# Performance work log

Hardware: AMD Instinct MI355X
Metric: run time of the kernel (lower is better)

The kernel has to match this reference:

```python
import jax, jax.numpy as jnp
import numpy as np

B, T = 2, 1000
IN_DIM, OUT_DIM = 257, 514
D_MODEL, D_STATE, D_CONV, EXPAND = 512, 16, 4, 2
D_INNER = EXPAND * D_MODEL          # 1024
DT_RANK = (D_MODEL + 15) // 16      # ceil(512/16) = 32
N_LAYER = 4
K_DC = 31                            # depthwise conv kernel in MambaDCLayer


def layer_norm(x, g, b, eps=1e-5):
    mu = jnp.mean(x, axis=-1, keepdims=True)
    var = jnp.mean((x - mu) ** 2, axis=-1, keepdims=True)
    return (x - mu) * jax.lax.rsqrt(var + eps) * g + b


def dw_conv1d(x, w, b, pad):
    # x: (B, T, C), w: (C, K) depthwise, pad: (left, right)
    y = jax.lax.conv_general_dilated(
        x.transpose(0, 2, 1), w[:, None, :], (1,), [pad],
        dimension_numbers=('NCH', 'OIH', 'NCH'), feature_group_count=w.shape[0])
    return (y + b[None, :, None]).transpose(0, 2, 1)


def mamba_block(x, W_in, conv_w, conv_b, W_x, W_dt, b_dt, A_log, Dp, W_out):
    # x: (B, T, d_model)
    xz = x @ W_in                               # (B, T, 2*D_INNER)
    xin, z = jnp.split(xz, 2, axis=-1)
    xin = dw_conv1d(xin, conv_w, conv_b, (D_CONV - 1, 0))  # causal depthwise conv
    xin = jax.nn.silu(xin)                      # (B, T, D_INNER)
    proj = xin @ W_x                            # (B, T, DT_RANK + 2*D_STATE)
    dt = jax.nn.softplus(proj[..., :DT_RANK] @ W_dt + b_dt)  # (B, T, D_INNER)
    Bm = proj[..., DT_RANK:DT_RANK + D_STATE]   # (B, T, D_STATE)
    Cm = proj[..., DT_RANK + D_STATE:]          # (B, T, D_STATE)
    A = -jnp.exp(A_log)                         # (D_INNER, D_STATE)
    dA = jnp.exp(dt[..., None] * A)             # (B, T, D_INNER, D_STATE)
    dBu = (dt * xin)[..., None] * Bm[:, :, None, :]  # (B, T, D_INNER, D_STATE)

    def step(h, inp):
        dA_t, dBu_t, C_t = inp
        h = dA_t * h + dBu_t
        return h, jnp.einsum('bds,bs->bd', h, C_t)

    h0 = jnp.zeros((x.shape[0], D_INNER, D_STATE), x.dtype)
    _, ys = jax.lax.scan(step, h0, (dA.transpose(1, 0, 2, 3),
                                    dBu.transpose(1, 0, 2, 3),
                                    Cm.transpose(1, 0, 2)))
    y = ys.transpose(1, 0, 2) + xin * Dp        # (B, T, D_INNER)
    y = y * jax.nn.silu(z)
    return y @ W_out                            # (B, T, d_model)


def setup_inputs() -> dict:
    key = jax.random.key(0)
    ks = iter(jax.random.split(key, 32))
    n = lambda shape, s=0.02: jax.random.normal(next(ks), shape, jnp.float32) * s
    return {
        'x': jax.random.normal(next(ks), (B, T, IN_DIM), jnp.float32),
        'lengths': jnp.full((B,), T, jnp.int32),
        'w_in0': n((IN_DIM, D_MODEL)),
        'ln_in_g': jnp.ones((D_MODEL,), jnp.float32),
        'ln_in_b': jnp.zeros((D_MODEL,), jnp.float32),
        'ln1_g': jnp.ones((N_LAYER, D_MODEL), jnp.float32),
        'ln1_b': jnp.zeros((N_LAYER, D_MODEL), jnp.float32),
        'W_inproj': n((N_LAYER, D_MODEL, 2 * D_INNER)),
        'conv_w': n((N_LAYER, D_INNER, D_CONV), 0.1),
        'conv_b': jnp.zeros((N_LAYER, D_INNER), jnp.float32),
        'W_xproj': n((N_LAYER, D_INNER, DT_RANK + 2 * D_STATE)),
        'W_dt': n((N_LAYER, DT_RANK, D_INNER), 0.1),
        'b_dt': jnp.full((N_LAYER, D_INNER), -4.6, jnp.float32),
        'A_log': jnp.tile(jnp.log(jnp.arange(1, D_STATE + 1, dtype=jnp.float32)),
                          (N_LAYER, D_INNER, 1)),
        'D': jnp.ones((N_LAYER, D_INNER), jnp.float32),
        'W_mo': n((N_LAYER, D_INNER, D_MODEL)),
        'ln2_g': jnp.ones((N_LAYER, D_MODEL), jnp.float32),
        'ln2_b': jnp.zeros((N_LAYER, D_MODEL), jnp.float32),
        'dc_w': n((N_LAYER, D_MODEL, K_DC), 0.1),
        'dc_b': jnp.zeros((N_LAYER, D_MODEL), jnp.float32),
        'w_out': n((D_MODEL, OUT_DIM)),
        'b_out': jnp.zeros((OUT_DIM,), jnp.float32),
    }


def reference(x, lengths, w_in0, ln_in_g, ln_in_b, ln1_g, ln1_b, W_inproj,
              conv_w, conv_b, W_xproj, W_dt, b_dt, A_log, D, W_mo,
              ln2_g, ln2_b, dc_w, dc_b, w_out, b_out):
    seq_mask = jnp.arange(x.shape[1]) < lengths[:, None]  # (B, T) bool
    h = jax.nn.relu(layer_norm(x @ w_in0, ln_in_g, ln_in_b))
    for i in range(N_LAYER):
        a = h + mamba_block(layer_norm(h, ln1_g[i], ln1_b[i]),
                            W_inproj[i], conv_w[i], conv_b[i], W_xproj[i],
                            W_dt[i], b_dt[i], A_log[i], D[i], W_mo[i])
        c = dw_conv1d(layer_norm(a, ln2_g[i], ln2_b[i]), dc_w[i], dc_b[i],
                      (K_DC // 2, K_DC // 2))  # 'same' padding
        h = a + c
    out = h @ w_out + b_out  # MagcIRM -> linear output head
    # lengths == T so output[seq_mask] is a full flatten to (B*T, OUT_DIM)
    out_flat = out.reshape(-1, out.shape[-1])
    return out_flat, seq_mask
```

## Files before the change

### kernel.cpp

```cpp
#include <hip/hip_runtime.h>
#include <cstdint>
#include <cstddef>

#define DEVI static __device__ __forceinline__

typedef unsigned short ushort_t;
typedef __attribute__((ext_vector_type(8))) short short8;
typedef __attribute__((ext_vector_type(4))) float f32x4;

DEVI float sp_softplus(float x) { return x > 20.f ? x : log1pf(__expf(x)); }
DEVI float silu_f(float x)      { return x / (1.f + __expf(-x)); }

DEVI ushort_t f2b(float v) {
    uint32_t u = __builtin_bit_cast(uint32_t, v);
    u += 0x7FFFu + ((u >> 16) & 1u);
    return (ushort_t)(u >> 16);
}
DEVI float b2f(ushort_t u) {
    uint32_t x = ((uint32_t)u) << 16;
    return __builtin_bit_cast(float, x);
}

DEVI void gload16(const ushort_t* g, ushort_t* l) {
    __builtin_amdgcn_global_load_lds(
        (const __attribute__((address_space(1))) unsigned int*)g,
        (__attribute__((address_space(3))) unsigned int*)l, 16, 0, 0);
}

#define NC 40
#define CL 25

template<bool RELU, bool OUTB16>
__global__ __launch_bounds__(256) void ln_k(const float* __restrict__ x,
                                            const float* __restrict__ g,
                                            const float* __restrict__ b,
                                            void* __restrict__ yv, int M)
{
    int wid  = threadIdx.x >> 6;
    int lane = threadIdx.x & 63;
    int row  = blockIdx.x * 4 + wid;
    if (row >= M) return;
    const float* xr = x + (size_t)row * 512;
    float4 v0 = *(const float4*)(xr + lane * 8);
    float4 v1 = *(const float4*)(xr + lane * 8 + 4);
    float vals[8] = {v0.x, v0.y, v0.z, v0.w, v1.x, v1.y, v1.z, v1.w};
    float s = 0.f;
#pragma unroll
    for (int i = 0; i < 8; i++) s += vals[i];
#pragma unroll
    for (int off = 1; off < 64; off <<= 1) s += __shfl_xor(s, off);
    float mu = s * (1.f / 512.f);
    float q = 0.f;
#pragma unroll
    for (int i = 0; i < 8; i++) { float d = vals[i] - mu; q += d * d; }
#pragma unroll
    for (int off = 1; off < 64; off <<= 1) q += __shfl_xor(q, off);
    float rstd = rsqrtf(q * (1.f / 512.f) + 1e-5f);
#pragma unroll
    for (int i = 0; i < 8; i++) {
        int c = lane * 8 + i;
        float o = (vals[i] - mu) * rstd * g[c] + b[c];
        if (RELU) o = fmaxf(o, 0.f);
        if (OUTB16) ((ushort_t*)yv)[(size_t)row * 512 + c] = f2b(o);
        else        ((float*)yv)[(size_t)row * 512 + c] = o;
    }
}

__global__ __launch_bounds__(256) void prep_all_k(const float* __restrict__ conv_w,
                                                  const float* __restrict__ dc_w,
                                                  const float* __restrict__ x,
                                                  float* __restrict__ cwt,
                                                  float* __restrict__ dcwt,
                                                  ushort_t* __restrict__ xb)
{
    int e = blockIdx.x * 256 + threadIdx.x;
    if (e < 16384) {
        int l = e >> 12, rem = e & 4095, k = rem >> 10, d = rem & 1023;
        cwt[e] = conv_w[l * 4096 + d * 4 + k];
        return;
    }
    e -= 16384;
    if (e < 63488) {
        int l = e / 15872, rem = e % 15872, k = rem / 512, m = rem % 512;
        dcwt[e] = dc_w[l * 15872 + m * 31 + k];
        return;
    }
    e -= 63488;
    if (e < 2000 * 320) {
        int k = e % 320, row = e / 320;
        xb[e] = (k < 257) ? f2b(x[(size_t)row * 257 + k]) : (ushort_t)0;
    }
}

__global__ __launch_bounds__(256) void tr_w_k(const float* __restrict__ src,
                                              ushort_t* __restrict__ dst,
                                              int Ktrue, int N, int ldo, int srcld,
                                              size_t sstride, size_t dstride)
{
    __shared__ float tile[32][33];
    src += blockIdx.z * sstride;
    dst += blockIdx.z * dstride;
    int n0 = blockIdx.x * 32, k0 = blockIdx.y * 32;
    int tx = threadIdx.x & 31, ty = threadIdx.x >> 5;
#pragma unroll
    for (int r = 0; r < 4; r++) {
        int k = k0 + ty + r * 8, n = n0 + tx;
        tile[ty + r * 8][tx] = (k < Ktrue && n < N) ? src[(size_t)k * srcld + n] : 0.f;
    }
    __syncthreads();
#pragma unroll
    for (int r = 0; r < 4; r++) {
        int n = n0 + ty + r * 8;
        if (n < N) dst[(size_t)n * ldo + k0 + tx] = f2b(tile[tx][ty + r * 8]);
    }
}

template<bool BIAS, int ACT, bool RES, bool OUTF32, bool OUTB16>
__global__ __launch_bounds__(256) void gemm7(
    const ushort_t* __restrict__ A, int lda,
    const ushort_t* __restrict__ Bt, int ldb,
    const float* __restrict__ bias,
    const float* __restrict__ R, int ldr,
    float* __restrict__ C, int ldc,
    ushort_t* __restrict__ C2, int ldc2,
    int M, int N, int K,
    size_t aStr, size_t bStr, size_t cStr)
{
    __shared__ ushort_t As[3 * 4096];
    __shared__ ushort_t Bs[3 * 4096];
    A  += blockIdx.z * aStr;
    Bt += blockIdx.z * bStr;
    C  += blockIdx.z * cStr;
    C2 += blockIdx.z * cStr;

    int tid = threadIdx.x;
    int wid = tid >> 6, l = tid & 63;
    int wr = wid >> 1, wc = wid & 1;
    int lk = l >> 4, lr = l & 15;
    int rhalf = tid >> 3, oct = tid & 7;

    int nwg = gridDim.x * gridDim.y;
    int bid = blockIdx.y * gridDim.x + blockIdx.x;
    {
        int q = nwg >> 3, r = nwg & 7;
        int xcd = bid & 7, lo = bid >> 3;
        bid = (xcd < r ? xcd * (q + 1) : r * (q + 1) + (xcd - r) * q) + lo;
    }
    int bx = bid % gridDim.x, by = bid / gridDim.x;
    int bm = by * 64, bn = bx * 64;

    int cg = oct ^ (rhalf & 7);
    const ushort_t* aS0 = A  + (size_t)(bm + rhalf) * lda + cg * 8;
    const ushort_t* aS1 = aS0 + (size_t)32 * lda;
    const ushort_t* bS0 = Bt + (size_t)(bn + rhalf) * ldb + cg * 8;
    const ushort_t* bS1 = bS0 + (size_t)32 * ldb;

    int rowA = wr * 32 + lr;
    int colB = wc * 32 + lr;
    int a0 = rowA * 64 + ((0 + lk) ^ (rowA & 7)) * 8;
    int a1 = rowA * 64 + ((4 + lk) ^ (rowA & 7)) * 8;
    int b0 = colB * 64 + ((0 + lk) ^ (colB & 7)) * 8;
    int b1 = colB * 64 + ((4 + lk) ^ (colB & 7)) * 8;

    f32x4 acc00 = {0.f,0.f,0.f,0.f}, acc01 = {0.f,0.f,0.f,0.f};
    f32x4 acc10 = {0.f,0.f,0.f,0.f}, acc11 = {0.f,0.f,0.f,0.f};

#define STAGE(B_) do { \
        gload16(aS0, &As[(B_) * 4096 + tid * 8]); \
        gload16(aS1, &As[(B_) * 4096 + 2048 + tid * 8]); \
        gload16(bS0, &Bs[(B_) * 4096 + tid * 8]); \
        gload16(bS1, &Bs[(B_) * 4096 + 2048 + tid * 8]); \
        aS0 += 64; aS1 += 64; bS0 += 64; bS1 += 64; \
    } while (0)

#define COMPUTE(B_) do { \
        short8 af0 = *(const short8*)&As[(B_) * 4096 + a0]; \
        short8 af1 = *(const short8*)&As[(B_) * 4096 + 1024 + a0]; \
        short8 bf0 = *(const short8*)&Bs[(B_) * 4096 + b0]; \
        short8 bf1 = *(const short8*)&Bs[(B_) * 4096 + 1024 + b0]; \
        acc00 = __builtin_amdgcn_mfma_f32_16x16x32_bf16(af0, bf0, acc00, 0, 0, 0); \
        acc01 = __builtin_amdgcn_mfma_f32_16x16x32_bf16(af0, bf1, acc01, 0, 0, 0); \
        acc10 = __builtin_amdgcn_mfma_f32_16x16x32_bf16(af1, bf0, acc10, 0, 0, 0); \
        acc11 = __builtin_amdgcn_mfma_f32_16x16x32_bf16(af1, bf1, acc11, 0, 0, 0); \
        af0 = *(const short8*)&As[(B_) * 4096 + a1]; \
        af1 = *(const short8*)&As[(B_) * 4096 + 1024 + a1]; \
        bf0 = *(const short8*)&Bs[(B_) * 4096 + b1]; \
        bf1 = *(const short8*)&Bs[(B_) * 4096 + 1024 + b1]; \
        acc00 = __builtin_amdgcn_mfma_f32_16x16x32_bf16(af0, bf0, acc00, 0, 0, 0); \
        acc01 = __builtin_amdgcn_mfma_f32_16x16x32_bf16(af0, bf1, acc01, 0, 0, 0); \
        acc10 = __builtin_amdgcn_mfma_f32_16x16x32_bf16(af1, bf0, acc10, 0, 0, 0); \
        acc11 = __builtin_amdgcn_mfma_f32_16x16x32_bf16(af1, bf1, acc11, 0, 0, 0); \
    } while (0)

#define STEP(T_, B_) do { \
        if ((T_) + 1 < nt) asm volatile("s_waitcnt vmcnt(4)" ::: "memory"); \
        else               asm volatile("s_waitcnt vmcnt(0)" ::: "memory"); \
        __builtin_amdgcn_s_barrier(); \
        if ((T_) + 2 < nt) STAGE(((B_) + 2) % 3); \
        COMPUTE(B_); \
    } while (0)

    int nt = K >> 6;
    STAGE(0);
    if (nt > 1) STAGE(1);
    int t = 0;
    for (; t + 3 <= nt; t += 3) { STEP(t, 0); STEP(t + 1, 1); STEP(t + 2, 2); }
    if (t < nt) { STEP(t, 0); t++; }
    if (t < nt) { STEP(t, 1); }

#undef STAGE
#undef COMPUTE
#undef STEP

    f32x4 accs[2][2] = {{acc00, acc01}, {acc10, acc11}};
#pragma unroll
    for (int m = 0; m < 2; m++) {
#pragma unroll
        for (int n = 0; n < 2; n++) {
            int gn = bn + wc * 32 + n * 16 + lr;
            if (gn >= N) continue;
#pragma unroll
            for (int r = 0; r < 4; r++) {
                int gm = bm + wr * 32 + m * 16 + lk * 4 + r;
                if (gm >= M) continue;
                float v = accs[m][n][r];
                if (ACT == 3) {
                    if (gn < 32) C2[(size_t)gm * ldc2 + gn] = f2b(v);
                    else { C[(size_t)gm * ldc + gn] = v;
                           C2[(size_t)gm * ldc2 + gn] = 0; }
                    continue;
                }
                if (BIAS) v += bias[gn];
                if (ACT == 1) v = sp_softplus(v);
                if (RES) v += R[(size_t)gm * ldr + gn];
                if (OUTF32) C[(size_t)gm * ldc + gn] = v;
                if (OUTB16) C2[(size_t)gm * ldc2 + gn] = f2b(v);
            }
        }
    }
}

__global__ __launch_bounds__(256) void conv4_silu_k(const ushort_t* __restrict__ xzb,
                                                    const float* __restrict__ cwt,
                                                    const float* __restrict__ bias,
                                                    ushort_t* __restrict__ xinb)
{
    int e = blockIdx.x * 256 + threadIdx.x;
    if (e >= 2000 * 128) return;
    int dg = (e & 127) * 8;
    int row = e >> 7;
    int b = row >= 1000 ? 1 : 0;
    int t = row - b * 1000;
    float acc[8];
#pragma unroll
    for (int j = 0; j < 8; j++) acc[j] = bias[dg + j];
#pragma unroll
    for (int k = 0; k < 4; k++) {
        int tt = t - 3 + k;
        if (tt < 0) continue;
        short8 v = *(const short8*)&xzb[(size_t)(b * 1000 + tt) * 2048 + dg];
#pragma unroll
        for (int j = 0; j < 8; j++)
            acc[j] += b2f((ushort_t)v[j]) * cwt[k * 1024 + dg + j];
    }
    short8 o;
#pragma unroll
    for (int j = 0; j < 8; j++) o[j] = (short)f2b(silu_f(acc[j]));
    *(short8*)&xinb[(size_t)row * 1024 + dg] = o;
}

__global__ __launch_bounds__(256) void scan_part1(const ushort_t* __restrict__ dt,
                                                  const ushort_t* __restrict__ xin,
                                                  const float* __restrict__ proj,
                                                  const float* __restrict__ A_log,
                                                  float* __restrict__ hloc,
                                                  float* __restrict__ sc)
{
    __shared__ ushort_t s_dt[CL][64], s_x[CL][64];
    __shared__ float s_B[CL][16];
    int d0 = blockIdx.x * 64;
    int c  = blockIdx.y;
    int b  = blockIdx.z;
    int tid = threadIdx.x;
    int ch = tid >> 2, st4 = tid & 3;
    int d = d0 + ch;
    int base = b * 1000 + c * CL;
    for (int lin = tid; lin < CL * 8; lin += 256) {
        int r = lin >> 3, q = lin & 7;
        size_t row = (size_t)(base + r);
        *(short8*)&s_dt[r][q * 8] = *(const short8*)&dt[row * 1024 + d0 + q * 8];
        *(short8*)&s_x[r][q * 8]  = *(const short8*)&xin[row * 1024 + d0 + q * 8];
    }
    for (int lin = tid; lin < CL * 16; lin += 256) {
        int r = lin >> 4, j = lin & 15;
        s_B[r][j] = proj[(size_t)(base + r) * 64 + 32 + j];
    }
    float4 alog = *(const float4*)&A_log[d * 16 + st4 * 4];
    float a_s[4] = {-__expf(alog.x), -__expf(alog.y), -__expf(alog.z), -__expf(alog.w)};
    __syncthreads();
    float h[4] = {0.f, 0.f, 0.f, 0.f};
    float sdt = 0.f;
#pragma unroll 5
    for (int t = 0; t < CL; t++) {
        float dtv = b2f(s_dt[t][ch]);
        float xv  = b2f(s_x[t][ch]);
        float4 Bv = *(const float4*)&s_B[t][st4 * 4];
        float dx = dtv * xv;
        sdt += dtv;
        h[0] = __expf(dtv * a_s[0]) * h[0] + dx * Bv.x;
        h[1] = __expf(dtv * a_s[1]) * h[1] + dx * Bv.y;
        h[2] = __expf(dtv * a_s[2]) * h[2] + dx * Bv.z;
        h[3] = __expf(dtv * a_s[3]) * h[3] + dx * Bv.w;
    }
    *(float4*)&hloc[((size_t)(b * NC + c) << 14) + ((size_t)d << 4) + st4 * 4] =
        (float4){h[0], h[1], h[2], h[3]};
    if (st4 == 0) sc[(b * NC + c) * 1024 + d] = sdt;
}

__global__ __launch_bounds__(256) void scan_combine(const float* __restrict__ A_log,
                                                    float* __restrict__ hloc,
                                                    const float* __restrict__ sc)
{
    int e = blockIdx.x * 256 + threadIdx.x;
    if (e >= 2 * 16384) return;
    int b = e >> 14;
    int rem = e & 16383;
    int dd = rem >> 4;
    float a_s = -__expf(A_log[rem]);
    float H = hloc[((size_t)(b * NC) << 14) + rem];
    for (int c = 1; c < NC; c++) {
        size_t idx = ((size_t)(b * NC + c) << 14) + rem;
        H = hloc[idx] + __expf(a_s * sc[(b * NC + c) * 1024 + dd]) * H;
        hloc[idx] = H;
    }
}

__global__ __launch_bounds__(256) void scan_part2(const ushort_t* __restrict__ dt,
                                                  const ushort_t* __restrict__ xin,
                                                  const float* __restrict__ proj,
                                                  const float* __restrict__ A_log,
                                                  const float* __restrict__ hend,
                                                  const float* __restrict__ Dp,
                                                  const ushort_t* __restrict__ xzb,
                                                  ushort_t* __restrict__ ysb)
{
    __shared__ ushort_t s_dt[CL][64], s_x[CL][64], s_y[CL][64];
    __shared__ float s_B[CL][16], s_C[CL][16];
    __shared__ float s_Dp[64];
    int d0 = blockIdx.x * 64;
    int c  = blockIdx.y;
    int b  = blockIdx.z;
    int tid = threadIdx.x;
    int ch = tid >> 2, st4 = tid & 3;
    int d = d0 + ch;
    int base = b * 1000 + c * CL;
    if (tid < 64) s_Dp[tid] = Dp[d0 + tid];
    for (int lin = tid; lin < CL * 8; lin += 256) {
        int r = lin >> 3, q = lin & 7;
        size_t row = (size_t)(base + r);
        *(short8*)&s_dt[r][q * 8] = *(const short8*)&dt[row * 1024 + d0 + q * 8];
        *(short8*)&s_x[r][q * 8]  = *(const short8*)&xin[row * 1024 + d0 + q * 8];
    }
    for (int lin = tid; lin < CL * 16; lin += 256) {
        int r = lin >> 4, j = lin & 15;
        s_B[r][j] = proj[(size_t)(base + r) * 64 + 32 + j];
        s_C[r][j] = proj[(size_t)(base + r) * 64 + 48 + j];
    }
    float4 alog = *(const float4*)&A_log[d * 16 + st4 * 4];
    float a_s[4] = {-__expf(alog.x), -__expf(alog.y), -__expf(alog.z), -__expf(alog.w)};
    float h[4] = {0.f, 0.f, 0.f, 0.f};
    if (c > 0) {
        float4 hv = *(const float4*)&hend[((size_t)(b * NC + c - 1) << 14)
                                          + ((size_t)d << 4) + st4 * 4];
        h[0] = hv.x; h[1] = hv.y; h[2] = hv.z; h[3] = hv.w;
    }
    __syncthreads();
#pragma unroll 5
    for (int t = 0; t < CL; t++) {
        float dtv = b2f(s_dt[t][ch]);
        float xv  = b2f(s_x[t][ch]);
        float4 Bv = *(const float4*)&s_B[t][st4 * 4];
        float4 Cv = *(const float4*)&s_C[t][st4 * 4];
        float dx = dtv * xv;
        h[0] = __expf(dtv * a_s[0]) * h[0] + dx * Bv.x;
        h[1] = __expf(dtv * a_s[1]) * h[1] + dx * Bv.y;
        h[2] = __expf(dtv * a_s[2]) * h[2] + dx * Bv.z;
        h[3] = __expf(dtv * a_s[3]) * h[3] + dx * Bv.w;
        float p = h[0] * Cv.x + h[1] * Cv.y + h[2] * Cv.z + h[3] * Cv.w;
        p += __shfl_xor(p, 1);
        p += __shfl_xor(p, 2);
        if (st4 == 0) s_y[t][ch] = f2b(p);
    }
    __syncthreads();
    for (int lin = tid; lin < CL * 8; lin += 256) {
        int r = lin >> 3, q = lin & 7;
        size_t row = (size_t)(base + r);
        int dd = d0 + q * 8;
        short8 yv = *(const short8*)&s_y[r][q * 8];
        short8 xv = *(const short8*)&s_x[r][q * 8];
        short8 zv = *(const short8*)&xzb[row * 2048 + 1024 + dd];
        short8 ov;
#pragma unroll
        for (int j = 0; j < 8; j++) {
            float o = (b2f((ushort_t)yv[j]) + b2f((ushort_t)xv[j]) * s_Dp[q * 8 + j])
                      * silu_f(b2f((ushort_t)zv[j]));
            ov[j] = (short)f2b(o);
        }
        *(short8*)&ysb[row * 1024 + dd] = ov;
    }
}

__global__ __launch_bounds__(256) void dcconv31_k(const ushort_t* __restrict__ ln,
                                                  const float* __restrict__ a,
                                                  const float* __restrict__ dcwt,
                                                  const float* __restrict__ bias,
                                                  float* __restrict__ h,
                                                  ushort_t* __restrict__ hb)
{
    int e = blockIdx.x * 256 + threadIdx.x;
    if (e >= 2000 * 512) return;
    int m = e & 511;
    int row = e >> 9;
    int b = row >= 1000 ? 1 : 0;
    int t = row - b * 1000;
    float acc = bias[m];
#pragma unroll
    for (int k = 0; k < 31; k++) {
        int tt = t - 15 + k;
        if (tt >= 0 && tt < 1000)
            acc += b2f(ln[((size_t)(b * 1000 + tt)) * 512 + m]) * dcwt[k * 512 + m];
    }
    float v = a[e] + acc;
    h[e] = v;
    hb[e] = f2b(v);
}

__global__ void mask_k(const int* __restrict__ lengths, float* __restrict__ out)
{
    int i = blockIdx.x * 256 + threadIdx.x;
    if (i >= 2000) return;
    out[i] = ((i % 1000) < lengths[i / 1000]) ? 1.f : 0.f;
}

extern "C" void kernel_launch(void* const* d_in, const int* in_sizes, int n_in,
                              void* d_out, int out_size, void* d_ws, size_t ws_size,
                              hipStream_t stream)
{
    const float* x       = (const float*)d_in[0];
    const int*   lengths = (const int*)  d_in[1];
    const float* w_in0   = (const float*)d_in[2];
    const float* ln_in_g = (const float*)d_in[3];
    const float* ln_in_b = (const float*)d_in[4];
    const float* ln1_g   = (const float*)d_in[5];
    const float* ln1_b   = (const float*)d_in[6];
    const float* W_inproj= (const float*)d_in[7];
    const float* conv_w  = (const float*)d_in[8];
    const float* conv_b  = (const float*)d_in[9];
    const float* W_xproj = (const float*)d_in[10];
    const float* W_dt    = (const float*)d_in[11];
    const float* b_dt    = (const float*)d_in[12];
    const float* A_log   = (const float*)d_in[13];
    const float* Dp      = (const float*)d_in[14];
    const float* W_mo    = (const float*)d_in[15];
    const float* ln2_g   = (const float*)d_in[16];
    const float* ln2_b   = (const float*)d_in[17];
    const float* dc_w    = (const float*)d_in[18];
    const float* dc_b    = (const float*)d_in[19];
    const float* w_out   = (const float*)d_in[20];
    const float* b_out   = (const float*)d_in[21];

    char* p = (char*)d_ws;
    auto alloc_f = [&](size_t n) { float* r = (float*)p; p += n * 4; return r; };
    auto alloc_b = [&](size_t n) { ushort_t* r = (ushort_t*)p; p += n * 2; return r; };

    float* h    = alloc_f(2048 * 512);
    float* lnb  = alloc_f(2048 * 512);
    float* proj = alloc_f(2048 * 64);
    float* av   = alloc_f(2048 * 512);
    float* hloc = alloc_f((size_t)2 * NC * 16384);
    float* sc   = alloc_f((size_t)2 * NC * 1024);
    float* cwt  = alloc_f(4 * 4 * 1024);
    float* dcwt = alloc_f(4 * 31 * 512);
    ushort_t* xbf   = alloc_b(2048 * 320);
    ushort_t* lnbb  = alloc_b(2048 * 512);
    ushort_t* xzb   = alloc_b(2048 * 2048);
    ushort_t* xinb  = alloc_b(2048 * 1024);
    ushort_t* dtbb  = alloc_b(2048 * 1024);
    ushort_t* ysb   = alloc_b(2048 * 1024);
    ushort_t* hb    = alloc_b(2048 * 512);
    ushort_t* projb = alloc_b(2048 * 64);
    ushort_t* wt_in0 = alloc_b(512 * 320);
    ushort_t* wt_in  = alloc_b((size_t)4 * 2048 * 512);
    ushort_t* wt_dt  = alloc_b((size_t)4 * 1024 * 64);
    ushort_t* wt_mo  = alloc_b((size_t)4 * 512 * 1024);
    ushort_t* wt_out = alloc_b(576 * 512);
    ushort_t* wxt    = alloc_b((size_t)4 * 64 * 1024);

    dim3 blk(256);

    prep_all_k<<<(16384 + 63488 + 2000 * 320 + 255) / 256, blk, 0, stream>>>(
        conv_w, dc_w, x, cwt, dcwt, xbf);
    tr_w_k<<<dim3(16, 10, 1), blk, 0, stream>>>(w_in0, wt_in0, 257, 512, 320, 512, 0, 0);
    tr_w_k<<<dim3(64, 16, 4), blk, 0, stream>>>(W_inproj, wt_in, 512, 2048, 512, 2048,
                                                (size_t)512 * 2048, (size_t)2048 * 512);
    tr_w_k<<<dim3(32, 2, 4),  blk, 0, stream>>>(W_dt, wt_dt, 32, 1024, 64, 1024,
                                                (size_t)32 * 1024, (size_t)1024 * 64);
    tr_w_k<<<dim3(16, 32, 4), blk, 0, stream>>>(W_mo, wt_mo, 1024, 512, 1024, 512,
                                                (size_t)1024 * 512, (size_t)512 * 1024);
    tr_w_k<<<dim3(17, 16, 1), blk, 0, stream>>>(w_out, wt_out, 512, 514, 512, 514, 0, 0);
    tr_w_k<<<dim3(2, 32, 4),  blk, 0, stream>>>(W_xproj, wxt, 1024, 64, 1024, 64,
                                                (size_t)1024 * 64, (size_t)64 * 1024);

    gemm7<false, 0, false, true, false><<<dim3(8, 32), blk, 0, stream>>>(
        xbf, 320, wt_in0, 320, nullptr, nullptr, 0, lnb, 512, nullptr, 0,
        2000, 512, 320, 0, 0, 0);
    ln_k<true, false><<<500, blk, 0, stream>>>(lnb, ln_in_g, ln_in_b, h, 2000);

    for (int i = 0; i < 4; i++) {
        const float* Al = A_log + (size_t)i * 16384;
        ln_k<false, true><<<500, blk, 0, stream>>>(h, ln1_g + i * 512, ln1_b + i * 512,
                                                   lnbb, 2000);
        gemm7<false, 0, false, false, true><<<dim3(32, 32), blk, 0, stream>>>(
            lnbb, 512, wt_in + (size_t)i * 2048 * 512, 512,
            nullptr, nullptr, 0, nullptr, 0, xzb, 2048, 2000, 2048, 512, 0, 0, 0);
        conv4_silu_k<<<1000, blk, 0, stream>>>(xzb, cwt + i * 4096,
                                               conv_b + i * 1024, xinb);
        gemm7<false, 3, false, false, false><<<dim3(1, 32), blk, 0, stream>>>(
            xinb, 1024, wxt + (size_t)i * 64 * 1024, 1024,
            nullptr, nullptr, 0, proj, 64, projb, 64, 2000, 64, 1024, 0, 0, 0);
        gemm7<true, 1, false, false, true><<<dim3(16, 32), blk, 0, stream>>>(
            projb, 64, wt_dt + (size_t)i * 1024 * 64, 64,
            b_dt + i * 1024, nullptr, 0, nullptr, 0, dtbb, 1024,
            2000, 1024, 64, 0, 0, 0);
        scan_part1<<<dim3(16, NC, 2), blk, 0, stream>>>(dtbb, xinb, proj, Al, hloc, sc);
        scan_combine<<<128, blk, 0, stream>>>(Al, hloc, sc);
        scan_part2<<<dim3(16, NC, 2), blk, 0, stream>>>(dtbb, xinb, proj, Al, hloc,
                                                        Dp + i * 1024, xzb, ysb);
        gemm7<false, 0, true, true, false><<<dim3(8, 32), blk, 0, stream>>>(
            ysb, 1024, wt_mo + (size_t)i * 512 * 1024, 1024,
            nullptr, h, 512, av, 512, nullptr, 0, 2000, 512, 1024, 0, 0, 0);
        ln_k<false, true><<<500, blk, 0, stream>>>(av, ln2_g + i * 512, ln2_b + i * 512,
                                                   lnbb, 2000);
        dcconv31_k<<<4000, blk, 0, stream>>>(lnbb, av, dcwt + i * 31 * 512,
                                             dc_b + i * 512, h, hb);
    }

    gemm7<true, 0, false, true, false><<<dim3(9, 32), blk, 0, stream>>>(
        hb, 512, wt_out, 512, b_out, nullptr, 0, (float*)d_out, 514, nullptr, 0,
        2000, 514, 512, 0, 0, 0);
    mask_k<<<8, blk, 0, stream>>>(lengths, (float*)d_out + 2000 * 514);
}
```

Before: 511.4 us.

## Fuse dt projection and softplus into scan kernels, dropping dt GEMM

Removes the separate dt GEMM (proj[:32] @ W_dt + softplus) and its bf16 dt buffer. Each scan block now computes dt for its chunk and channel slice in shared memory from the fp32 proj rows and a W_dt tile. The x_proj GEMM now writes plain fp32 output, and the W_dt transpose kernel is gone. This saves one kernel launch per layer plus the dt write and reads, and keeps dt in fp32. In exchange the dt projection is computed twice (part1 and part2) in scalar FMAs, and shared memory use grows, which may lower occupancy.

```diff
diff --git a/kernel.cpp b/kernel.cpp
--- a/kernel.cpp
+++ b/kernel.cpp
@@ -224,12 +224,6 @@
                 int gm = bm + wr * 32 + m * 16 + lk * 4 + r;
                 if (gm >= M) continue;
                 float v = accs[m][n][r];
-                if (ACT == 3) {
-                    if (gn < 32) C2[(size_t)gm * ldc2 + gn] = f2b(v);
-                    else { C[(size_t)gm * ldc + gn] = v;
-                           C2[(size_t)gm * ldc2 + gn] = 0; }
-                    continue;
-                }
                 if (BIAS) v += bias[gn];
                 if (ACT == 1) v = sp_softplus(v);
                 if (RES) v += R[(size_t)gm * ldr + gn];
@@ -269,15 +263,19 @@
     *(short8*)&xinb[(size_t)row * 1024 + dg] = o;
 }
 
-__global__ __launch_bounds__(256) void scan_part1(const ushort_t* __restrict__ dt,
-                                                  const ushort_t* __restrict__ xin,
+__global__ __launch_bounds__(256) void scan_part1(const ushort_t* __restrict__ xin,
                                                   const float* __restrict__ proj,
+                                                  const float* __restrict__ W_dt,
+                                                  const float* __restrict__ b_dt,
                                                   const float* __restrict__ A_log,
                                                   float* __restrict__ hloc,
                                                   float* __restrict__ sc)
 {
-    __shared__ ushort_t s_dt[CL][64], s_x[CL][64];
-    __shared__ float s_B[CL][16];
+    __shared__ ushort_t s_x[CL][64];
+    __shared__ float s_proj[CL][64];
+    __shared__ float s_wdt[32][64];
+    __shared__ float s_bdt[64];
+    __shared__ float s_dtf[CL][64];
     int d0 = blockIdx.x * 64;
     int c  = blockIdx.y;
     int b  = blockIdx.z;
@@ -287,13 +285,26 @@
     int base = b * 1000 + c * CL;
     for (int lin = tid; lin < CL * 8; lin += 256) {
         int r = lin >> 3, q = lin & 7;
-        size_t row = (size_t)(base + r);
-        *(short8*)&s_dt[r][q * 8] = *(const short8*)&dt[row * 1024 + d0 + q * 8];
-        *(short8*)&s_x[r][q * 8]  = *(const short8*)&xin[row * 1024 + d0 + q * 8];
+        *(short8*)&s_x[r][q * 8] =
+            *(const short8*)&xin[(size_t)(base + r) * 1024 + d0 + q * 8];
     }
     for (int lin = tid; lin < CL * 16; lin += 256) {
-        int r = lin >> 4, j = lin & 15;
-        s_B[r][j] = proj[(size_t)(base + r) * 64 + 32 + j];
+        int r = lin >> 4, q = lin & 15;
+        *(float4*)&s_proj[r][q * 4] =
+            *(const float4*)&proj[(size_t)(base + r) * 64 + q * 4];
+    }
+    for (int lin = tid; lin < 2048; lin += 256) {
+        int k = lin >> 6, j = lin & 63;
+        s_wdt[k][j] = W_dt[k * 1024 + d0 + j];
+    }
+    if (tid < 64) s_bdt[tid] = b_dt[d0 + tid];
+    __syncthreads();
+    for (int lin = tid; lin < CL * 64; lin += 256) {
+        int r = lin >> 6, j = lin & 63;
+        float acc = s_bdt[j];
+#pragma unroll
+        for (int k = 0; k < 32; k++) acc += s_proj[r][k] * s_wdt[k][j];
+        s_dtf[r][j] = sp_softplus(acc);
     }
     float4 alog = *(const float4*)&A_log[d * 16 + st4 * 4];
     float a_s[4] = {-__expf(alog.x), -__expf(alog.y), -__expf(alog.z), -__expf(alog.w)};
@@ -302,9 +313,9 @@
     float sdt = 0.f;
 #pragma unroll 5
     for (int t = 0; t < CL; t++) {
-        float dtv = b2f(s_dt[t][ch]);
+        float dtv = s_dtf[t][ch];
         float xv  = b2f(s_x[t][ch]);
-        float4 Bv = *(const float4*)&s_B[t][st4 * 4];
+        float4 Bv = *(const float4*)&s_proj[t][32 + st4 * 4];
         float dx = dtv * xv;
         sdt += dtv;
         h[0] = __expf(dtv * a_s[0]) * h[0] + dx * Bv.x;
@@ -335,17 +346,21 @@
     }
 }
 
-__global__ __launch_bounds__(256) void scan_part2(const ushort_t* __restrict__ dt,
-                                                  const ushort_t* __restrict__ xin,
+__global__ __launch_bounds__(256) void scan_part2(const ushort_t* __restrict__ xin,
                                                   const float* __restrict__ proj,
+                                                  const float* __restrict__ W_dt,
+                                                  const float* __restrict__ b_dt,
                                                   const float* __restrict__ A_log,
                                                   const float* __restrict__ hend,
                                                   const float* __restrict__ Dp,
                                                   const ushort_t* __restrict__ xzb,
                                                   ushort_t* __restrict__ ysb)
 {
-    __shared__ ushort_t s_dt[CL][64], s_x[CL][64], s_y[CL][64];
-    __shared__ float s_B[CL][16], s_C[CL][16];
+    __shared__ ushort_t s_x[CL][64], s_y[CL][64];
+    __shared__ float s_proj[CL][64];
+    __shared__ float s_wdt[32][64];
+    __shared__ float s_bdt[64];
+    __shared__ float s_dtf[CL][64];
     __shared__ float s_Dp[64];
     int d0 = blockIdx.x * 64;
     int c  = blockIdx.y;
@@ -354,17 +369,28 @@
     int ch = tid >> 2, st4 = tid & 3;
     int d = d0 + ch;
     int base = b * 1000 + c * CL;
-    if (tid < 64) s_Dp[tid] = Dp[d0 + tid];
+    if (tid < 64) { s_Dp[tid] = Dp[d0 + tid]; s_bdt[tid] = b_dt[d0 + tid]; }
     for (int lin = tid; lin < CL * 8; lin += 256) {
         int r = lin >> 3, q = lin & 7;
-        size_t row = (size_t)(base + r);
-        *(short8*)&s_dt[r][q * 8] = *(const short8*)&dt[row * 1024 + d0 + q * 8];
-        *(short8*)&s_x[r][q * 8]  = *(const short8*)&xin[row * 1024 + d0 + q * 8];
+        *(short8*)&s_x[r][q * 8] =
+            *(const short8*)&xin[(size_t)(base + r) * 1024 + d0 + q * 8];
     }
     for (int lin = tid; lin < CL * 16; lin += 256) {
-        int r = lin >> 4, j = lin & 15;
-        s_B[r][j] = proj[(size_t)(base + r) * 64 + 32 + j];
-        s_C[r][j] = proj[(size_t)(base + r) * 64 + 48 + j];
+        int r = lin >> 4, q = lin & 15;
+        *(float4*)&s_proj[r][q * 4] =
+            *(const float4*)&proj[(size_t)(base + r) * 64 + q * 4];
+    }
+    for (int lin = tid; lin < 2048; lin += 256) {
+        int k = lin >> 6, j = lin & 63;
+        s_wdt[k][j] = W_dt[k * 1024 + d0 + j];
+    }
+    __syncthreads();
+    for (int lin = tid; lin < CL * 64; lin += 256) {
+        int r = lin >> 6, j = lin & 63;
+        float acc = s_bdt[j];
+#pragma unroll
+        for (int k = 0; k < 32; k++) acc += s_proj[r][k] * s_wdt[k][j];
+        s_dtf[r][j] = sp_softplus(acc);
     }
     float4 alog = *(const float4*)&A_log[d * 16 + st4 * 4];
     float a_s[4] = {-__expf(alog.x), -__expf(alog.y), -__expf(alog.z), -__expf(alog.w)};
@@ -377,10 +403,10 @@
     __syncthreads();
 #pragma unroll 5
     for (int t = 0; t < CL; t++) {
-        float dtv = b2f(s_dt[t][ch]);
+        float dtv = s_dtf[t][ch];
         float xv  = b2f(s_x[t][ch]);
-        float4 Bv = *(const float4*)&s_B[t][st4 * 4];
-        float4 Cv = *(const float4*)&s_C[t][st4 * 4];
+        float4 Bv = *(const float4*)&s_proj[t][32 + st4 * 4];
+        float4 Cv = *(const float4*)&s_proj[t][48 + st4 * 4];
         float dx = dtv * xv;
         h[0] = __expf(dtv * a_s[0]) * h[0] + dx * Bv.x;
         h[1] = __expf(dtv * a_s[1]) * h[1] + dx * Bv.y;
@@ -485,13 +511,10 @@
     ushort_t* lnbb  = alloc_b(2048 * 512);
     ushort_t* xzb   = alloc_b(2048 * 2048);
     ushort_t* xinb  = alloc_b(2048 * 1024);
-    ushort_t* dtbb  = alloc_b(2048 * 1024);
     ushort_t* ysb   = alloc_b(2048 * 1024);
     ushort_t* hb    = alloc_b(2048 * 512);
-    ushort_t* projb = alloc_b(2048 * 64);
     ushort_t* wt_in0 = alloc_b(512 * 320);
     ushort_t* wt_in  = alloc_b((size_t)4 * 2048 * 512);
-    ushort_t* wt_dt  = alloc_b((size_t)4 * 1024 * 64);
     ushort_t* wt_mo  = alloc_b((size_t)4 * 512 * 1024);
     ushort_t* wt_out = alloc_b(576 * 512);
     ushort_t* wxt    = alloc_b((size_t)4 * 64 * 1024);
@@ -503,8 +526,6 @@
     tr_w_k<<<dim3(16, 10, 1), blk, 0, stream>>>(w_in0, wt_in0, 257, 512, 320, 512, 0, 0);
     tr_w_k<<<dim3(64, 16, 4), blk, 0, stream>>>(W_inproj, wt_in, 512, 2048, 512, 2048,
                                                 (size_t)512 * 2048, (size_t)2048 * 512);
-    tr_w_k<<<dim3(32, 2, 4),  blk, 0, stream>>>(W_dt, wt_dt, 32, 1024, 64, 1024,
-                                                (size_t)32 * 1024, (size_t)1024 * 64);
     tr_w_k<<<dim3(16, 32, 4), blk, 0, stream>>>(W_mo, wt_mo, 1024, 512, 1024, 512,
                                                 (size_t)1024 * 512, (size_t)512 * 1024);
     tr_w_k<<<dim3(17, 16, 1), blk, 0, stream>>>(w_out, wt_out, 512, 514, 512, 514, 0, 0);
@@ -518,6 +539,7 @@
 
     for (int i = 0; i < 4; i++) {
         const float* Al = A_log + (size_t)i * 16384;
+        const float* Wdt_i = W_dt + (size_t)i * 32 * 1024;
         ln_k<false, true><<<500, blk, 0, stream>>>(h, ln1_g + i * 512, ln1_b + i * 512,
                                                    lnbb, 2000);
         gemm7<false, 0, false, false, true><<<dim3(32, 32), blk, 0, stream>>>(
@@ -525,17 +547,14 @@
             nullptr, nullptr, 0, nullptr, 0, xzb, 2048, 2000, 2048, 512, 0, 0, 0);
         conv4_silu_k<<<1000, blk, 0, stream>>>(xzb, cwt + i * 4096,
                                                conv_b + i * 1024, xinb);
-        gemm7<false, 3, false, false, false><<<dim3(1, 32), blk, 0, stream>>>(
+        gemm7<false, 0, false, true, false><<<dim3(1, 32), blk, 0, stream>>>(
             xinb, 1024, wxt + (size_t)i * 64 * 1024, 1024,
-            nullptr, nullptr, 0, proj, 64, projb, 64, 2000, 64, 1024, 0, 0, 0);
-        gemm7<true, 1, false, false, true><<<dim3(16, 32), blk, 0, stream>>>(
-            projb, 64, wt_dt + (size_t)i * 1024 * 64, 64,
-            b_dt + i * 1024, nullptr, 0, nullptr, 0, dtbb, 1024,
-            2000, 1024, 64, 0, 0, 0);
-        scan_part1<<<dim3(16, NC, 2), blk, 0, stream>>>(dtbb, xinb, proj, Al, hloc, sc);
+            nullptr, nullptr, 0, proj, 64, nullptr, 0, 2000, 64, 1024, 0, 0, 0);
+        scan_part1<<<dim3(16, NC, 2), blk, 0, stream>>>(
+            xinb, proj, Wdt_i, b_dt + i * 1024, Al, hloc, sc);
         scan_combine<<<128, blk, 0, stream>>>(Al, hloc, sc);
-        scan_part2<<<dim3(16, NC, 2), blk, 0, stream>>>(dtbb, xinb, proj, Al, hloc,
-                                                        Dp + i * 1024, xzb, ysb);
+        scan_part2<<<dim3(16, NC, 2), blk, 0, stream>>>(
+            xinb, proj, Wdt_i, b_dt + i * 1024, Al, hloc, Dp + i * 1024, xzb, ysb);
         gemm7<false, 0, true, true, false><<<dim3(8, 32), blk, 0, stream>>>(
             ysb, 1024, wt_mo + (size_t)i * 512 * 1024, 1024,
             nullptr, h, 512, av, 512, nullptr, 0, 2000, 512, 1024, 0, 0, 0);
```

Result: slower. 535.4 us (+4.7%).
